# Optimization experiments

Hardware: AMD Instinct MI355X
Metric: run time of the kernel (lower is better)

Reference implementation:

```python
import jax, jax.numpy as jnp
import numpy as np

BATCH_SIZE = 4096
DIM = 128
TEMPERATURE = 0.5
EPS = 1e-8


def setup_inputs() -> dict:
    key = jax.random.key(0)
    k1, k2 = jax.random.split(key)
    z_i = jax.random.normal(k1, (BATCH_SIZE, DIM), dtype=jnp.float32)
    z_j = jax.random.normal(k2, (BATCH_SIZE, DIM), dtype=jnp.float32)
    return {"z_i": z_i, "z_j": z_j}


def reference(z_i, z_j):
    B = z_i.shape[0]
    N = 2 * B
    z = jnp.concatenate([z_i, z_j], axis=0)  # [N, D]
    # cosine similarity = matmul of L2-normalized rows (avoids the NxNxD broadcast)
    zn = z / jnp.maximum(jnp.linalg.norm(z, axis=1, keepdims=True), EPS)
    sim = (zn @ zn.T) / TEMPERATURE  # [N, N]
    idx = jnp.arange(N)
    # positive pair: row i pairs with row (i+B) mod N (covers both diag offsets +B and -B)
    pos = sim[idx, (idx + B) % N]  # [N]
    # CE over logits [pos, negatives]; the logit set per row is the full sim row
    # minus the self-similarity (diagonal). Mask diagonal with a large negative.
    neg_inf = jnp.asarray(-1e9, sim.dtype)
    sim_masked = jnp.where(idx[:, None] == idx[None, :], neg_inf, sim)
    lse = jax.nn.logsumexp(sim_masked, axis=1)  # [N]
    # CrossEntropyLoss(reduction='sum') with label 0 (the positive), divided by N
    loss = jnp.sum(lse - pos) / N
    return loss
```

## Files before the change

kernel.cpp:

```cpp
#include <hip/hip_runtime.h>
#include <cstdint>


#define BROWS 4096
#define NROWS 8192
#define ROWB  256
#define CSPL  24
#define CT32  256
#define BRT   256
#define TILEB 8192

typedef __attribute__((ext_vector_type(8))) __bf16    bf16x8;
typedef __attribute__((ext_vector_type(4))) float     f32x4;
typedef __attribute__((ext_vector_type(4))) uint32_t  u32x4;

#define K1F 2.8853900817779268f
#define LN2F 0.69314718055994531f
#define BC8(x) __builtin_bit_cast(bf16x8, x)

__device__ __forceinline__ uint16_t f2bf(float f) {
    uint32_t u = __builtin_bit_cast(uint32_t, f);
    u = (u + 0x7FFFu + ((u >> 16) & 1u)) >> 16;
    return (uint16_t)u;
}
__device__ __forceinline__ float bf2f(uint16_t b) {
    return __builtin_bit_cast(float, ((uint32_t)b) << 16);
}
__device__ __forceinline__ void gload_lds16(const void* g, void* l) {
    __builtin_amdgcn_global_load_lds(
        (const __attribute__((address_space(1))) void*)g,
        (__attribute__((address_space(3))) void*)l, 16, 0, 0);
}

__global__ __launch_bounds__(256) void k_normalize(
    const float* __restrict__ zi, const float* __restrict__ zj,
    uint16_t* __restrict__ znA, uint16_t* __restrict__ znB)
{
    int tid  = threadIdx.x;
    int lane = tid & 63;
    int wid  = tid >> 6;
    int li   = lane & 7;
    int row  = blockIdx.x * 32 + wid * 8 + (lane >> 3);

    const float* src = (row < BROWS) ? (zi + (size_t)row * 128)
                                     : (zj + (size_t)(row - BROWS) * 128);
    float4 v[4];
    const float4* s4 = (const float4*)(src + li * 16);
#pragma unroll
    for (int c = 0; c < 4; ++c) v[c] = s4[c];

    float ss = 0.f;
#pragma unroll
    for (int c = 0; c < 4; ++c)
        ss += v[c].x*v[c].x + v[c].y*v[c].y + v[c].z*v[c].z + v[c].w*v[c].w;
#pragma unroll
    for (int off = 1; off < 8; off <<= 1) ss += __shfl_xor(ss, off);

    float scale = 1.0f / fmaxf(sqrtf(ss), 1e-8f);

    float e[16];
#pragma unroll
    for (int c = 0; c < 4; ++c) {
        e[c*4+0] = v[c].x * scale; e[c*4+1] = v[c].y * scale;
        e[c*4+2] = v[c].z * scale; e[c*4+3] = v[c].w * scale;
    }
    uint32_t wB[8], wA[8];
#pragma unroll
    for (int q = 0; q < 8; ++q) {
        wB[q] = (uint32_t)f2bf(e[2*q])       | ((uint32_t)f2bf(e[2*q+1])       << 16);
        wA[q] = (uint32_t)f2bf(e[2*q] * K1F) | ((uint32_t)f2bf(e[2*q+1] * K1F) << 16);
    }
    uint4* dB = (uint4*)((char*)znB + (size_t)row * ROWB + li * 32);
    dB[0] = make_uint4(wB[0], wB[1], wB[2], wB[3]);
    dB[1] = make_uint4(wB[4], wB[5], wB[6], wB[7]);
    uint4* dA = (uint4*)((char*)znA + (size_t)row * ROWB + li * 32);
    dA[0] = make_uint4(wA[0], wA[1], wA[2], wA[3]);
    dA[1] = make_uint4(wA[4], wA[5], wA[6], wA[7]);
}

__global__ __launch_bounds__(256)
__attribute__((amdgpu_waves_per_eu(3, 3)))
void k_simlse(
    const uint16_t* __restrict__ znA, const uint16_t* __restrict__ znB,
    float* __restrict__ partial)
{
    __shared__ __align__(16) char lds[3][TILEB];

    const char* zA = (const char*)znA;
    const char* zB = (const char*)znB;
    int tid  = threadIdx.x;
    int lane = tid & 63;
    int wid  = tid >> 6;
    int lo16 = lane & 15;
    int hi4  = lane >> 4;
    int rowBase = blockIdx.x * BRT + wid * 64;

    u32x4 a[4][4];
#pragma unroll
    for (int rt = 0; rt < 4; ++rt) {
        const char* ap = zA + (size_t)(rowBase + rt * 16 + lo16) * ROWB + hi4 * 16;
#pragma unroll
        for (int kf = 0; kf < 4; ++kf)
            a[rt][kf] = *(const u32x4*)(ap + kf * 64);
    }

    float rs[4][4];
#pragma unroll
    for (int rt = 0; rt < 4; ++rt)
#pragma unroll
        for (int r = 0; r < 4; ++r) rs[rt][r] = 0.f;

    int t0 = (CT32 * blockIdx.y) / CSPL;
    int t1 = (CT32 * (blockIdx.y + 1)) / CSPL;
    int nt = t1 - t0;

    const char* gsrc = zB + (size_t)t0 * TILEB
                     + ((tid * 16) ^ (((tid >> 4) & 7) << 4));
    int xorv = (lo16 & 7) << 4;

#define STAGE(sel, t) do {                                                     \
        const char* g_ = gsrc + (size_t)(t) * TILEB;                           \
        gload_lds16(g_,        &lds[sel][wid * 1024]);                         \
        gload_lds16(g_ + 4096, &lds[sel][4096 + wid * 1024]);                  \
    } while (0)

#define COMPUTE(sel) do {                                                        \
        _Pragma("unroll")                                                        \
        for (int ct = 0; ct < 2; ++ct) {                                         \
            const char* lb_ = &lds[sel][ct * 4096 + lo16 * 256];                 \
            u32x4 bf[4];                                                         \
            _Pragma("unroll")                                                    \
            for (int kf = 0; kf < 4; ++kf)                                       \
                bf[kf] = *(const u32x4*)(lb_ + ((hi4 * 16 + kf * 64) ^ xorv));   \
            f32x4 ac0 = {0.f,0.f,0.f,0.f}, ac1 = {0.f,0.f,0.f,0.f};              \
            f32x4 ac2 = {0.f,0.f,0.f,0.f}, ac3 = {0.f,0.f,0.f,0.f};              \
            _Pragma("unroll")                                                    \
            for (int kf = 0; kf < 4; ++kf) {                                     \
                bf16x8 bk_ = BC8(bf[kf]);                                        \
                ac0 = __builtin_amdgcn_mfma_f32_16x16x32_bf16(BC8(a[0][kf]), bk_, ac0, 0, 0, 0); \
                ac1 = __builtin_amdgcn_mfma_f32_16x16x32_bf16(BC8(a[1][kf]), bk_, ac1, 0, 0, 0); \
                ac2 = __builtin_amdgcn_mfma_f32_16x16x32_bf16(BC8(a[2][kf]), bk_, ac2, 0, 0, 0); \
                ac3 = __builtin_amdgcn_mfma_f32_16x16x32_bf16(BC8(a[3][kf]), bk_, ac3, 0, 0, 0); \
            }                                                                    \
            _Pragma("unroll")                                                    \
            for (int r = 0; r < 4; ++r) {                                        \
                rs[0][r] += __builtin_amdgcn_exp2f(ac0[r]);                      \
                rs[1][r] += __builtin_amdgcn_exp2f(ac1[r]);                      \
                rs[2][r] += __builtin_amdgcn_exp2f(ac2[r]);                      \
                rs[3][r] += __builtin_amdgcn_exp2f(ac3[r]);                      \
            }                                                                    \
        }                                                                        \
    } while (0)

    STAGE(0, 0);
    STAGE(1, 1);

    int t = 0;
    for (; t < nt - 1; ++t) {
        asm volatile("s_waitcnt vmcnt(2)" ::: "memory");
        __builtin_amdgcn_s_barrier();
        __builtin_amdgcn_sched_barrier(0);
        COMPUTE(t % 3);
        if (t + 2 < nt) STAGE((t + 2) % 3, t + 2);
    }
    asm volatile("s_waitcnt vmcnt(0)" ::: "memory");
    __builtin_amdgcn_s_barrier();
    __builtin_amdgcn_sched_barrier(0);
    COMPUTE(t % 3);

#undef STAGE
#undef COMPUTE

#pragma unroll
    for (int rt = 0; rt < 4; ++rt)
#pragma unroll
        for (int r = 0; r < 4; ++r) {
            float s = rs[rt][r];
            s += __shfl_xor(s, 1);  s += __shfl_xor(s, 2);
            s += __shfl_xor(s, 4);  s += __shfl_xor(s, 8);
            if (lo16 == 0) {
                int row = rowBase + rt * 16 + hi4 * 4 + r;
                partial[blockIdx.y * NROWS + row] = s;
            }
        }
}

__global__ __launch_bounds__(256) void k_finalize(
    const uint16_t* __restrict__ znA, const uint16_t* __restrict__ znB,
    const float* __restrict__ partial, float* __restrict__ blocksum)
{
    int tid = threadIdx.x;
    int i = blockIdx.x * 256 + tid;

    float S = 0.f;
#pragma unroll
    for (int cs = 0; cs < CSPL; ++cs) S += partial[cs * NROWS + i];

    int j = (i + BROWS) & (NROWS - 1);
    const uint4* rAi = (const uint4*)((const char*)znA + (size_t)i * ROWB);
    const uint4* rBi = (const uint4*)((const char*)znB + (size_t)i * ROWB);
    const uint4* rBj = (const uint4*)((const char*)znB + (size_t)j * ROWB);
    float adot = 0.f;
    float sdot = 0.f;
#pragma unroll
    for (int c = 0; c < 16; ++c) {
        uint4 ua = rAi[c], ub = rBi[c], vb = rBj[c];
        const uint32_t* pa = (const uint32_t*)&ua;
        const uint32_t* pb = (const uint32_t*)&ub;
        const uint32_t* pv = (const uint32_t*)&vb;
#pragma unroll
        for (int q = 0; q < 4; ++q) {
            float a0 = bf2f((uint16_t)(pa[q] & 0xffffu)), a1 = bf2f((uint16_t)(pa[q] >> 16));
            float b0 = bf2f((uint16_t)(pb[q] & 0xffffu)), b1 = bf2f((uint16_t)(pb[q] >> 16));
            float v0 = bf2f((uint16_t)(pv[q] & 0xffffu)), v1 = bf2f((uint16_t)(pv[q] >> 16));
            adot += a0 * v0 + a1 * v1;
            sdot += a0 * b0 + a1 * b1;
        }
    }
    S -= __builtin_amdgcn_exp2f(sdot);
    float c = LN2F * (__builtin_amdgcn_logf(S) - adot);

#pragma unroll
    for (int off = 1; off < 64; off <<= 1) c += __shfl_xor(c, off);
    __shared__ float wsum[4];
    int lane = tid & 63, wid = tid >> 6;
    if (lane == 0) wsum[wid] = c;
    __syncthreads();
    if (tid == 0) blocksum[blockIdx.x] = wsum[0] + wsum[1] + wsum[2] + wsum[3];
}

__global__ __launch_bounds__(64) void k_reduce(
    const float* __restrict__ blocksum, float* __restrict__ out)
{
    int tid = threadIdx.x;
    float v = (tid < 32) ? blocksum[tid] : 0.f;
#pragma unroll
    for (int off = 1; off < 64; off <<= 1) v += __shfl_xor(v, off);
    if (tid == 0) out[0] = v * (1.0f / (float)NROWS);
}

extern "C" void kernel_launch(void* const* d_in, const int* in_sizes, int n_in,
                              void* d_out, int out_size, void* d_ws, size_t ws_size,
                              hipStream_t stream)
{
    const float* zi = (const float*)d_in[0];
    const float* zj = (const float*)d_in[1];
    float* out = (float*)d_out;

    char* ws = (char*)d_ws;
    uint16_t* znA      = (uint16_t*)ws;
    uint16_t* znB      = (uint16_t*)(ws + (size_t)NROWS * ROWB);
    float*    partial  = (float*)(ws + 2 * (size_t)NROWS * ROWB);
    float*    blocksum = (float*)(ws + 2 * (size_t)NROWS * ROWB
                                     + (size_t)CSPL * NROWS * 4);

    k_normalize<<<dim3(256), dim3(256), 0, stream>>>(zi, zj, znA, znB);
    k_simlse  <<<dim3(32, CSPL), dim3(256), 0, stream>>>(znA, znB, partial);
    k_finalize<<<dim3(32), dim3(256), 0, stream>>>(znA, znB, partial, blocksum);
    k_reduce  <<<dim3(1), dim3(64), 0, stream>>>(blocksum, out);
}
```

Baseline: 39.09 us.

## Software-pipeline MFMA with exp accumulation and deepen LDS ring to four stages

The LDS tile ring grows from three to four buffers, so three tiles are in flight ahead of compute. The compute loop is restructured so the exp2/accumulate for one column tile runs interleaved with the MFMAs of the next, keeping MFMA and VALU work overlapped. This costs more LDS per block and more live accumulator registers, which may pressure occupancy under the fixed waves_per_eu setting.

Measured after the change: 40.01 us. 1.02x slower.

```diff
diff --git a/kernel.cpp b/kernel.cpp
--- a/kernel.cpp
+++ b/kernel.cpp
@@ -84,7 +84,7 @@
     const uint16_t* __restrict__ znA, const uint16_t* __restrict__ znB,
     float* __restrict__ partial)
 {
-    __shared__ __align__(16) char lds[3][TILEB];
+    __shared__ __align__(16) char lds[4][TILEB];
 
     const char* zA = (const char*)znA;
     const char* zB = (const char*)znB;
@@ -124,52 +124,91 @@
         gload_lds16(g_ + 4096, &lds[sel][4096 + wid * 1024]);                  \
     } while (0)
 
-#define COMPUTE(sel) do {                                                        \
-        _Pragma("unroll")                                                        \
-        for (int ct = 0; ct < 2; ++ct) {                                         \
-            const char* lb_ = &lds[sel][ct * 4096 + lo16 * 256];                 \
-            u32x4 bf[4];                                                         \
-            _Pragma("unroll")                                                    \
-            for (int kf = 0; kf < 4; ++kf)                                       \
-                bf[kf] = *(const u32x4*)(lb_ + ((hi4 * 16 + kf * 64) ^ xorv));   \
-            f32x4 ac0 = {0.f,0.f,0.f,0.f}, ac1 = {0.f,0.f,0.f,0.f};              \
-            f32x4 ac2 = {0.f,0.f,0.f,0.f}, ac3 = {0.f,0.f,0.f,0.f};              \
-            _Pragma("unroll")                                                    \
-            for (int kf = 0; kf < 4; ++kf) {                                     \
-                bf16x8 bk_ = BC8(bf[kf]);                                        \
-                ac0 = __builtin_amdgcn_mfma_f32_16x16x32_bf16(BC8(a[0][kf]), bk_, ac0, 0, 0, 0); \
-                ac1 = __builtin_amdgcn_mfma_f32_16x16x32_bf16(BC8(a[1][kf]), bk_, ac1, 0, 0, 0); \
-                ac2 = __builtin_amdgcn_mfma_f32_16x16x32_bf16(BC8(a[2][kf]), bk_, ac2, 0, 0, 0); \
-                ac3 = __builtin_amdgcn_mfma_f32_16x16x32_bf16(BC8(a[3][kf]), bk_, ac3, 0, 0, 0); \
-            }                                                                    \
-            _Pragma("unroll")                                                    \
-            for (int r = 0; r < 4; ++r) {                                        \
-                rs[0][r] += __builtin_amdgcn_exp2f(ac0[r]);                      \
-                rs[1][r] += __builtin_amdgcn_exp2f(ac1[r]);                      \
-                rs[2][r] += __builtin_amdgcn_exp2f(ac2[r]);                      \
-                rs[3][r] += __builtin_amdgcn_exp2f(ac3[r]);                      \
-            }                                                                    \
-        }                                                                        \
+#define MFMA_CT(sel, ct, D0, D1, D2, D3) do {                                  \
+        const char* lb_ = &lds[sel][(ct) * 4096 + lo16 * 256];                 \
+        u32x4 bf0 = *(const u32x4*)(lb_ + ((hi4 * 16 +   0) ^ xorv));          \
+        u32x4 bf1 = *(const u32x4*)(lb_ + ((hi4 * 16 +  64) ^ xorv));          \
+        u32x4 bf2 = *(const u32x4*)(lb_ + ((hi4 * 16 + 128) ^ xorv));          \
+        u32x4 bf3 = *(const u32x4*)(lb_ + ((hi4 * 16 + 192) ^ xorv));          \
+        D0 = (f32x4){0.f,0.f,0.f,0.f}; D1 = (f32x4){0.f,0.f,0.f,0.f};          \
+        D2 = (f32x4){0.f,0.f,0.f,0.f}; D3 = (f32x4){0.f,0.f,0.f,0.f};          \
+        D0 = __builtin_amdgcn_mfma_f32_16x16x32_bf16(BC8(a[0][0]), BC8(bf0), D0, 0, 0, 0); \
+        D1 = __builtin_amdgcn_mfma_f32_16x16x32_bf16(BC8(a[1][0]), BC8(bf0), D1, 0, 0, 0); \
+        D2 = __builtin_amdgcn_mfma_f32_16x16x32_bf16(BC8(a[2][0]), BC8(bf0), D2, 0, 0, 0); \
+        D3 = __builtin_amdgcn_mfma_f32_16x16x32_bf16(BC8(a[3][0]), BC8(bf0), D3, 0, 0, 0); \
+        D0 = __builtin_amdgcn_mfma_f32_16x16x32_bf16(BC8(a[0][1]), BC8(bf1), D0, 0, 0, 0); \
+        D1 = __builtin_amdgcn_mfma_f32_16x16x32_bf16(BC8(a[1][1]), BC8(bf1), D1, 0, 0, 0); \
+        D2 = __builtin_amdgcn_mfma_f32_16x16x32_bf16(BC8(a[2][1]), BC8(bf1), D2, 0, 0, 0); \
+        D3 = __builtin_amdgcn_mfma_f32_16x16x32_bf16(BC8(a[3][1]), BC8(bf1), D3, 0, 0, 0); \
+        D0 = __builtin_amdgcn_mfma_f32_16x16x32_bf16(BC8(a[0][2]), BC8(bf2), D0, 0, 0, 0); \
+        D1 = __builtin_amdgcn_mfma_f32_16x16x32_bf16(BC8(a[1][2]), BC8(bf2), D1, 0, 0, 0); \
+        D2 = __builtin_amdgcn_mfma_f32_16x16x32_bf16(BC8(a[2][2]), BC8(bf2), D2, 0, 0, 0); \
+        D3 = __builtin_amdgcn_mfma_f32_16x16x32_bf16(BC8(a[3][2]), BC8(bf2), D3, 0, 0, 0); \
+        D0 = __builtin_amdgcn_mfma_f32_16x16x32_bf16(BC8(a[0][3]), BC8(bf3), D0, 0, 0, 0); \
+        D1 = __builtin_amdgcn_mfma_f32_16x16x32_bf16(BC8(a[1][3]), BC8(bf3), D1, 0, 0, 0); \
+        D2 = __builtin_amdgcn_mfma_f32_16x16x32_bf16(BC8(a[2][3]), BC8(bf3), D2, 0, 0, 0); \
+        D3 = __builtin_amdgcn_mfma_f32_16x16x32_bf16(BC8(a[3][3]), BC8(bf3), D3, 0, 0, 0); \
     } while (0)
 
-    STAGE(0, 0);
-    STAGE(1, 1);
-
-    int t = 0;
-    for (; t < nt - 1; ++t) {
-        asm volatile("s_waitcnt vmcnt(2)" ::: "memory");
-        __builtin_amdgcn_s_barrier();
-        __builtin_amdgcn_sched_barrier(0);
-        COMPUTE(t % 3);
-        if (t + 2 < nt) STAGE((t + 2) % 3, t + 2);
-    }
-    asm volatile("s_waitcnt vmcnt(0)" ::: "memory");
-    __builtin_amdgcn_s_barrier();
-    __builtin_amdgcn_sched_barrier(0);
-    COMPUTE(t % 3);
+#define EXPADD(P0, P1, P2, P3) do {                                            \
+        _Pragma("unroll")                                                      \
+        for (int r = 0; r < 4; ++r) {                                          \
+            rs[0][r] += __builtin_amdgcn_exp2f(P0[r]);                         \
+            rs[1][r] += __builtin_amdgcn_exp2f(P1[r]);                         \
+            rs[2][r] += __builtin_amdgcn_exp2f(P2[r]);                         \
+            rs[3][r] += __builtin_amdgcn_exp2f(P3[r]);                         \
+        }                                                                      \
+    } while (0)
+
+#define WAITBAR(n) do {                                                       \
+        asm volatile("s_waitcnt vmcnt(" #n ")" ::: "memory");                  \
+        __builtin_amdgcn_s_barrier();                                          \
+        __builtin_amdgcn_sched_barrier(0);                                     \
+    } while (0)
+
+    f32x4 cc0, cc1, cc2, cc3;
+    f32x4 pa0, pa1, pa2, pa3;
+
+    STAGE(0, 0); STAGE(1, 1); STAGE(2, 2);
+
+    WAITBAR(4);
+    MFMA_CT(0, 0, cc0, cc1, cc2, cc3);
+    MFMA_CT(0, 1, pa0, pa1, pa2, pa3);
+    EXPADD(cc0, cc1, cc2, cc3);
+    STAGE(3, 3);
+
+    int t = 1;
+    for (; t < nt - 2; ++t) {
+        WAITBAR(4);
+        int sel = t & 3;
+        MFMA_CT(sel, 0, cc0, cc1, cc2, cc3);
+        EXPADD(pa0, pa1, pa2, pa3);
+        MFMA_CT(sel, 1, pa0, pa1, pa2, pa3);
+        EXPADD(cc0, cc1, cc2, cc3);
+        if (t + 3 < nt) STAGE((t + 3) & 3, t + 3);
+    }
+    WAITBAR(2);
+    {
+        int sel = (nt - 2) & 3;
+        MFMA_CT(sel, 0, cc0, cc1, cc2, cc3);
+        EXPADD(pa0, pa1, pa2, pa3);
+        MFMA_CT(sel, 1, pa0, pa1, pa2, pa3);
+        EXPADD(cc0, cc1, cc2, cc3);
+    }
+    WAITBAR(0);
+    {
+        int sel = (nt - 1) & 3;
+        MFMA_CT(sel, 0, cc0, cc1, cc2, cc3);
+        EXPADD(pa0, pa1, pa2, pa3);
+        MFMA_CT(sel, 1, pa0, pa1, pa2, pa3);
+        EXPADD(cc0, cc1, cc2, cc3);
+    }
+    EXPADD(pa0, pa1, pa2, pa3);
 
 #undef STAGE
-#undef COMPUTE
+#undef MFMA_CT
+#undef EXPADD
+#undef WAITBAR
 
 #pragma unroll
     for (int rt = 0; rt < 4; ++rt)
```
